# Optimization experiments

Hardware: AMD Instinct MI355X
Metric: run time of the kernel (lower is better)

Reference implementation:

```python
import jax, jax.numpy as jnp
import numpy as np


def setup_inputs() -> dict:
    key = jax.random.key(0)
    ks = jax.random.split(key, 6)
    B, C, H, W, Q = 16, 64, 64, 64, 8192
    HID = 256
    K = C * 9  # 576, unfolded channel count and srnet out_dim (co_mat=1)
    feat = jax.random.normal(ks[0], (B, C, H, W), jnp.float32)
    coord = jax.random.uniform(ks[1], (B, Q, 2), jnp.float32) * 2.0 - 1.0  # normalized [-1,1]
    cell = jnp.ones((B, Q, 2), jnp.float32) * (2.0 / 128.0)  # HR cell size for 128-px grid
    w1 = jax.random.normal(ks[2], (3, HID), jnp.float32) / np.sqrt(3.0)
    b1 = jnp.zeros((HID,), jnp.float32)
    w2 = jax.random.normal(ks[3], (HID, HID), jnp.float32) / np.sqrt(float(HID))
    b2 = jnp.zeros((HID,), jnp.float32)
    w3 = jax.random.normal(ks[4], (HID, K), jnp.float32) / np.sqrt(float(HID))
    b3 = jnp.zeros((K,), jnp.float32)
    return {"feat": feat, "coord": coord, "cell": cell,
            "w1": w1, "b1": b1, "w2": w2, "b2": b2, "w3": w3, "b3": b3}


def reference(feat, coord, cell, w1, b1, w2, b2, w3, b3):
    B, C, H, W = feat.shape
    Q = coord.shape[1]
    K = C * 9
    co_mat = 1
    # F.unfold(feat, 3, padding=1).view(B, C*9, H, W): channel-major, kernel pos minor
    padded = jnp.pad(feat, ((0, 0), (0, 0), (1, 1), (1, 1)))
    patches = jnp.stack([padded[:, :, i:i + H, j:j + W]
                         for i in range(3) for j in range(3)], axis=2)  # [B,C,9,H,W]
    featu = patches.reshape(B, K, H * W)
    # shift query coords by half a cell
    coord_ = coord - cell / 2.0
    coord_q = jnp.clip(coord_ + 1e-6, -1.0 + 1e-6, 1.0 - 1e-6)
    # nearest grid_sample, align_corners=False: idx = round(((c+1)*S - 1)/2)
    # coord[...,0] indexes H (grid y after flip), coord[...,1] indexes W (grid x)
    iy = jnp.clip(jnp.round(((coord_q[..., 0] + 1.0) * H - 1.0) / 2.0), 0, H - 1).astype(jnp.int32)
    ix = jnp.clip(jnp.round(((coord_q[..., 1] + 1.0) * W - 1.0) / 2.0), 0, W - 1).astype(jnp.int32)
    lin = iy * W + ix  # [B,Q]
    q_feat = jnp.take_along_axis(featu, lin[:, None, :], axis=2).transpose(0, 2, 1)  # [B,Q,K]
    # q_coord: make_coord value minus half-pixel shift at the nearest index = 2i/S - 1 (exact)
    qy = 2.0 * iy.astype(jnp.float32) / H - 1.0
    qx = 2.0 * ix.astype(jnp.float32) / W - 1.0
    rel_y = (coord_[..., 0] - qy) * (H / 2.0)
    rel_x = (coord_[..., 1] - qx) * (W / 2.0)
    r_rev = cell[..., 0] * (H / 2.0)
    inp = jnp.stack([rel_y, rel_x, r_rev], axis=-1)  # [B,Q,3]
    # srnet MLP: per-query filter of shape [K, co_mat]
    h = jax.nn.relu(inp @ w1 + b1)
    h = jax.nn.relu(h @ w2 + b2)
    wmat = (h @ w3 + b3).reshape(B, Q, K, co_mat)
    # bmm combine: [1,K] @ [K,co_mat] per query
    pred = jnp.einsum('bqk,bqkc->bqc', q_feat, wmat)  # [B,Q,1]
    return pred
```

## Files before the change

kernel.cpp:

```cpp
#include <hip/hip_runtime.h>
#include <hip/hip_bf16.h>

#define BB 16
#define CC 64
#define HH 64
#define WW 64
#define QQ 8192
#define HID 256
#define KK 576
#define HT 66
#define FROW 264

typedef short short8 __attribute__((ext_vector_type(8)));
typedef short sv4    __attribute__((ext_vector_type(4)));
typedef float f32x4  __attribute__((ext_vector_type(4)));

__device__ __forceinline__ short f2bf(float f) {
    union { float f; unsigned u; } v; v.f = f;
    unsigned r = v.u + 0x7fffu + ((v.u >> 16) & 1u);
    return (short)(r >> 16);
}
__device__ __forceinline__ float bf2f(short s) {
    union { unsigned u; float f; } v; v.u = ((unsigned)(unsigned short)s) << 16;
    return v.f;
}
__device__ __forceinline__ void barrier_lds() {
    asm volatile("s_waitcnt lgkmcnt(0)" ::: "memory");
    __builtin_amdgcn_s_barrier();
    asm volatile("" ::: "memory");
}
__device__ __forceinline__ void glld16(const short* g, short* l) {
    __builtin_amdgcn_global_load_lds(
        (const __attribute__((address_space(1))) void*)g,
        (__attribute__((address_space(3))) void*)l, 16, 0, 0);
}

__global__ __launch_bounds__(256) void prep_transpose_k(const float* __restrict__ feat,
                                                        const float* __restrict__ w2,
                                                        const float* __restrict__ w3,
                                                        const float* __restrict__ b3,
                                                        short* __restrict__ featT,
                                                        short* __restrict__ w3cB,
                                                        short* __restrict__ w2cB) {
    __shared__ float ftile[64][65];
    const int t = threadIdx.x;
    const int gidx = blockIdx.x * 256 + t;

    if (gidx < 156672) {
        int kchunk = gidx / 2176;
        int rem = gidx - kchunk * 2176;
        int n = rem >> 3, j = rem & 7;
        int kglob = kchunk * 8 + j;
        int pos = kglob >> 6, c = kglob & 63;
        float v = 0.f;
        if (n < 256)      v = w3[n * KK + c * 9 + pos];
        else if (n == 256) v = b3[c * 9 + pos];
        w3cB[gidx] = f2bf(v);
    }
    if (gidx < 65536) {
        int kchunk = gidx >> 11;
        int rem = gidx & 2047;
        int n = rem >> 3, j = rem & 7;
        int k = kchunk * 8 + j;
        w2cB[gidx] = f2bf(w2[k * 256 + n]);
    }

    const int b = blockIdx.x / HT;
    const int yy = blockIdx.x - b * HT;
    short* out_row = featT + ((b * HT + yy) * HT) * 64;

    if (yy == 0 || yy == HT - 1) {
        for (int idx = t; idx < HT * 64; idx += 256) out_row[idx] = 0;
        return;
    }
    const int y = yy - 1;
    const float* src = feat + ((b * CC) * HH + y) * WW;
#pragma unroll
    for (int i = 0; i < 16; ++i) {
        int idx = i * 256 + t;
        int c = idx >> 6, x = idx & 63;
        ftile[c][x] = src[c * (HH * WW) + x];
    }
    if (t < 64) out_row[t] = 0;
    else if (t < 128) out_row[(HT - 1) * 64 + (t - 64)] = 0;
    __syncthreads();
#pragma unroll
    for (int i = 0; i < 16; ++i) {
        int idx = i * 256 + t;
        int x = idx >> 6, c = idx & 63;
        out_row[(x + 1) * 64 + c] = f2bf(ftile[c][x]);
    }
}

#define SSTR 72
__global__ __launch_bounds__(256, 2) void conv_k(const short* __restrict__ featT,
                                                 const short* __restrict__ w3cB,
                                                 short* __restrict__ F) {
    __shared__ short slab[3 * HT * SSTR];
    __shared__ short Bb[2][8704];
    const int t = threadIdx.x;
    const int wave = t >> 6, lane = t & 63, quad = lane >> 4, ln16 = lane & 15;
    const int b = blockIdx.x >> 6, y = blockIdx.x & 63;

    f32x4 acc[4][5];
#pragma unroll
    for (int a = 0; a < 4; ++a)
#pragma unroll
        for (int i = 0; i < 5; ++i) acc[a][i] = (f32x4){0.f, 0.f, 0.f, 0.f};

    auto stageB = [&](int buf, int st) {
        const short* src = w3cB + st * 8704;
#pragma unroll
        for (int u = 0; u < 5; ++u) {
            int cidx = (u < 4) ? (u * 4 + wave) : 16;
            if (u < 4 || wave == 0)
                glld16(src + cidx * 512 + lane * 8, &Bb[buf][cidx * 512]);
        }
    };

    stageB(0, 0);

    const short* slabsrc = featT + b * (HT * HT * 64) + y * (HT * 64);
#pragma unroll
    for (int it = 0; it < 7; ++it) {
        int i = it * 256 + t;
        if (i < 1584) {
            short8 v = *(const short8*)(slabsrc + i * 8);
            int row = i >> 3, cs = (i & 7) * 8;
            *(short8*)(&slab[row * SSTR + cs]) = v;
        }
    }
    __syncthreads();

#pragma unroll
    for (int st = 0; st < 18; ++st) {
        const int cur = st & 1;
        if (st < 17) stageB(cur ^ 1, st + 1);
        const int pos = st >> 1, ks = st & 1;
        const int di = pos / 3, dj = pos - di * 3;
        short8 af[4];
#pragma unroll
        for (int ms = 0; ms < 4; ++ms)
            af[ms] = *(const short8*)(&slab[(di * HT + ms * 16 + ln16 + dj) * SSTR + ks * 32 + quad * 8]);
#pragma unroll
        for (int i = 0; i < 5; ++i) {
            int sub = (i < 4) ? (wave + 4 * i) : 16;
            short8 bf = *(const short8*)(&Bb[cur][(quad * 272 + sub * 16 + ln16) * 8]);
#pragma unroll
            for (int ms = 0; ms < 4; ++ms)
                acc[ms][i] = __builtin_amdgcn_mfma_f32_16x16x32_bf16(af[ms], bf, acc[ms][i], 0, 0, 0);
        }
        __syncthreads();
    }

#pragma unroll
    for (int h = 0; h < 2; ++h) {
#pragma unroll
        for (int i = 0; i < 5; ++i) {
            int sub = (i < 4) ? (wave + 4 * i) : 16;
            int n = sub * 16 + ln16;
            bool store = (i < 4) || (wave == 0 && n < FROW);
            if (store) {
#pragma unroll
                for (int ms2 = 0; ms2 < 2; ++ms2) {
                    int ms = h * 2 + ms2;
#pragma unroll
                    for (int r = 0; r < 4; ++r) {
                        int xl = ms2 * 16 + quad * 4 + r;
                        slab[xl * FROW + n] = f2bf(acc[ms][i][r]);
                    }
                }
            }
        }
        __syncthreads();
        short8* dst = (short8*)(F + ((long)(b * 64 + y) * 64 + h * 32) * FROW);
        const short8* src8 = (const short8*)slab;
#pragma unroll
        for (int it = 0; it < 5; ++it) {
            int idx = it * 256 + t;
            if (idx < (32 * FROW) / 8) dst[idx] = src8[idx];
        }
        __syncthreads();
    }
}

#define HSTR 264
__global__ __launch_bounds__(256, 3) void mlp_k(const float* __restrict__ coord,
                                                const float* __restrict__ cell,
                                                const float* __restrict__ w1,
                                                const float* __restrict__ b1,
                                                const float* __restrict__ b2v,
                                                const short* __restrict__ w2cB,
                                                const short* __restrict__ F,
                                                float* __restrict__ out) {
    __shared__ short Hh[64 * HSTR];
    __shared__ float red_s[64][4];

    const int t = threadIdx.x;
    const int wave = t >> 6, lane = t & 63, quad = lane >> 4, ln16 = lane & 15;
    const int qbase = blockIdx.x * 64;
    const int b = qbase >> 13;

    short8 wbuf[3][4];
    const short* w2base = w2cB + (quad * 256 + wave * 64 + ln16) * 8;
    auto loadW = [&](int s, int slot) {
#pragma unroll
        for (int i = 0; i < 4; ++i)
            wbuf[slot][i] = *(const short8*)(w2base + s * 8192 + i * 128);
    };

    const int g = qbase + lane;
    const float2 cc = *(const float2*)(coord + g * 2);
    const float2 ce = *(const float2*)(cell + g * 2);

    loadW(0, 0);
    loadW(1, 1);

    const float coy = cc.x - ce.x * 0.5f, cox = cc.y - ce.y * 0.5f;
    const float cqy = fminf(fmaxf(coy + 1e-6f, -0.999999f), 0.999999f);
    const float cqx = fminf(fmaxf(cox + 1e-6f, -0.999999f), 0.999999f);
    int iy = (int)rintf(((cqy + 1.0f) * 64.0f - 1.0f) * 0.5f); iy = min(max(iy, 0), 63);
    int ix = (int)rintf(((cqx + 1.0f) * 64.0f - 1.0f) * 0.5f); ix = min(max(ix, 0), 63);
    const int lin = iy * 64 + ix;
    const float in0 = (coy - ((float)iy * (1.0f / 32.0f) - 1.0f)) * 32.0f;
    const float in1 = (cox - ((float)ix * (1.0f / 32.0f) - 1.0f)) * 32.0f;
    const float in2 = ce.x * 32.0f;

    int linm[4];
#pragma unroll
    for (int ms = 0; ms < 4; ++ms) linm[ms] = __shfl(lin, ms * 16 + ln16, 64);

    short8 hv[8];
    const int k0w = wave * 64;
#pragma unroll
    for (int c8 = 0; c8 < 8; ++c8) {
        const int k0 = k0w + c8 * 8;
        f32x4 wa0 = *(const f32x4*)(w1 + k0),       wa1 = *(const f32x4*)(w1 + k0 + 4);
        f32x4 wb0 = *(const f32x4*)(w1 + 256 + k0), wb1 = *(const f32x4*)(w1 + 256 + k0 + 4);
        f32x4 wc0 = *(const f32x4*)(w1 + 512 + k0), wc1 = *(const f32x4*)(w1 + 512 + k0 + 4);
        f32x4 bb0 = *(const f32x4*)(b1 + k0),       bb1 = *(const f32x4*)(b1 + k0 + 4);
#pragma unroll
        for (int jj = 0; jj < 4; ++jj) {
            float v0 = fmaf(in0, wa0[jj], fmaf(in1, wb0[jj], fmaf(in2, wc0[jj], bb0[jj])));
            float v1 = fmaf(in0, wa1[jj], fmaf(in1, wb1[jj], fmaf(in2, wc1[jj], bb1[jj])));
            hv[c8][jj]     = f2bf(fmaxf(v0, 0.f));
            hv[c8][jj + 4] = f2bf(fmaxf(v1, 0.f));
        }
    }
#pragma unroll
    for (int c8 = 0; c8 < 8; ++c8)
        *(short8*)(&Hh[lane * HSTR + wave * 64 + c8 * 8]) = hv[c8];
    barrier_lds();

    const short* Fb = F + (long)b * 4096 * FROW;
    sv4 fv[4][4];
    short fbs = 0;
    f32x4 b2q[4];
    f32x4 acc2[4][4];
#pragma unroll
    for (int i = 0; i < 4; ++i)
#pragma unroll
        for (int ms = 0; ms < 4; ++ms) acc2[i][ms] = (f32x4){0.f, 0.f, 0.f, 0.f};

#pragma unroll
    for (int s = 0; s < 8; ++s) {
        if (s < 6) loadW(s + 2, (s + 2) % 3);
        short8 hf[4];
#pragma unroll
        for (int ms = 0; ms < 4; ++ms)
            hf[ms] = *(const short8*)(&Hh[(ms * 16 + ln16) * HSTR + s * 32 + quad * 8]);
        if (s == 6) {
#pragma unroll
            for (int ms = 0; ms < 4; ++ms) {
                const short* Fr = Fb + (long)linm[ms] * FROW + wave * 64 + quad * 4;
#pragma unroll
                for (int i = 0; i < 4; ++i) fv[ms][i] = *(const sv4*)(Fr + i * 16);
            }
            fbs = Fb[(long)lin * FROW + 256];
        }
        if (s == 7) {
#pragma unroll
            for (int i = 0; i < 4; ++i)
                b2q[i] = *(const f32x4*)(b2v + wave * 64 + i * 16 + quad * 4);
        }
#pragma unroll
        for (int i = 0; i < 4; ++i)
#pragma unroll
            for (int ms = 0; ms < 4; ++ms)
                acc2[i][ms] = __builtin_amdgcn_mfma_f32_16x16x32_bf16(wbuf[s % 3][i], hf[ms], acc2[i][ms], 0, 0, 0);
    }

    const float fbv = bf2f(fbs);
    float part[4] = {0.f, 0.f, 0.f, 0.f};
#pragma unroll
    for (int i = 0; i < 4; ++i)
#pragma unroll
        for (int ms = 0; ms < 4; ++ms)
#pragma unroll
            for (int r = 0; r < 4; ++r)
                part[ms] = fmaf(fmaxf(acc2[i][ms][r] + b2q[i][r], 0.f), bf2f(fv[ms][i][r]), part[ms]);
#pragma unroll
    for (int ms = 0; ms < 4; ++ms) {
        part[ms] += __shfl_xor(part[ms], 16, 64);
        part[ms] += __shfl_xor(part[ms], 32, 64);
    }
    if (quad == 0) {
#pragma unroll
        for (int ms = 0; ms < 4; ++ms) red_s[ms * 16 + ln16][wave] = part[ms];
    }
    barrier_lds();
    if (t < 64)
        out[qbase + t] = red_s[t][0] + red_s[t][1] + red_s[t][2] + red_s[t][3] + fbv;
}

extern "C" void kernel_launch(void* const* d_in, const int* in_sizes, int n_in,
                              void* d_out, int out_size, void* d_ws, size_t ws_size,
                              hipStream_t stream) {
    const float* feat  = (const float*)d_in[0];
    const float* coord = (const float*)d_in[1];
    const float* cell  = (const float*)d_in[2];
    const float* w1    = (const float*)d_in[3];
    const float* b1    = (const float*)d_in[4];
    const float* w2    = (const float*)d_in[5];
    const float* b2    = (const float*)d_in[6];
    const float* w3    = (const float*)d_in[7];
    const float* b3    = (const float*)d_in[8];
    float* out = (float*)d_out;

    char* ws = (char*)d_ws;
    short* w3cB  = (short*)(ws);
    short* w2cB  = (short*)(ws + 313344);
    short* featT = (short*)(ws + 444416);
    short* F     = (short*)(ws + 9365504);
    (void)ws_size; (void)in_sizes; (void)n_in; (void)out_size;

    prep_transpose_k<<<BB * HT, 256, 0, stream>>>(feat, w2, w3, b3, featT, w3cB, w2cB);
    conv_k<<<BB * HH, 256, 0, stream>>>(featT, w3cB, F);
    mlp_k<<<(BB * QQ) / 64, 256, 0, stream>>>(coord, cell, w1, b1, b2, w2cB, F, out);
}
```

Before: 150.9 us.

## Load conv B operand straight into registers with triple-buffered prefetch

In the conv kernel, the w3-derived B fragments are no longer staged through a double-buffered LDS array via global_load_lds. Each lane now loads its own short8 fragments from global memory into a three-slot register ring, prefetching two stages ahead. This removes the per-stage __syncthreads and about 35 KB of LDS per block. The cost is roughly 60 extra VGPRs, which risks spills under the two-blocks-per-SM launch bound. Dropping the last main-loop barrier also leaves a possible race: a wave may start writing the epilogue into slab while another wave is still reading its final A fragments from slab.

```diff
diff --git a/kernel.cpp b/kernel.cpp
--- a/kernel.cpp
+++ b/kernel.cpp
@@ -28,11 +28,6 @@
     asm volatile("s_waitcnt lgkmcnt(0)" ::: "memory");
     __builtin_amdgcn_s_barrier();
     asm volatile("" ::: "memory");
-}
-__device__ __forceinline__ void glld16(const short* g, short* l) {
-    __builtin_amdgcn_global_load_lds(
-        (const __attribute__((address_space(1))) void*)g,
-        (__attribute__((address_space(3))) void*)l, 16, 0, 0);
 }
 
 __global__ __launch_bounds__(256) void prep_transpose_k(const float* __restrict__ feat,
@@ -97,7 +92,6 @@
                                                  const short* __restrict__ w3cB,
                                                  short* __restrict__ F) {
     __shared__ short slab[3 * HT * SSTR];
-    __shared__ short Bb[2][8704];
     const int t = threadIdx.x;
     const int wave = t >> 6, lane = t & 63, quad = lane >> 4, ln16 = lane & 15;
     const int b = blockIdx.x >> 6, y = blockIdx.x & 63;
@@ -108,17 +102,18 @@
 #pragma unroll
         for (int i = 0; i < 5; ++i) acc[a][i] = (f32x4){0.f, 0.f, 0.f, 0.f};
 
-    auto stageB = [&](int buf, int st) {
-        const short* src = w3cB + st * 8704;
-#pragma unroll
-        for (int u = 0; u < 5; ++u) {
-            int cidx = (u < 4) ? (u * 4 + wave) : 16;
-            if (u < 4 || wave == 0)
-                glld16(src + cidx * 512 + lane * 8, &Bb[buf][cidx * 512]);
+    short8 bbuf[3][5];
+    const short* bbase = w3cB + (quad * 272 + ln16) * 8;
+    auto loadB = [&](int st, int slot) {
+#pragma unroll
+        for (int i = 0; i < 5; ++i) {
+            int sub = (i < 4) ? (wave + 4 * i) : 16;
+            bbuf[slot][i] = *(const short8*)(bbase + st * 8704 + sub * 128);
         }
     };
 
-    stageB(0, 0);
+    loadB(0, 0);
+    loadB(1, 1);
 
     const short* slabsrc = featT + b * (HT * HT * 64) + y * (HT * 64);
 #pragma unroll
@@ -130,12 +125,11 @@
             *(short8*)(&slab[row * SSTR + cs]) = v;
         }
     }
-    __syncthreads();
+    barrier_lds();
 
 #pragma unroll
     for (int st = 0; st < 18; ++st) {
-        const int cur = st & 1;
-        if (st < 17) stageB(cur ^ 1, st + 1);
+        if (st < 16) loadB(st + 2, (st + 2) % 3);
         const int pos = st >> 1, ks = st & 1;
         const int di = pos / 3, dj = pos - di * 3;
         short8 af[4];
@@ -143,18 +137,15 @@
         for (int ms = 0; ms < 4; ++ms)
             af[ms] = *(const short8*)(&slab[(di * HT + ms * 16 + ln16 + dj) * SSTR + ks * 32 + quad * 8]);
 #pragma unroll
-        for (int i = 0; i < 5; ++i) {
-            int sub = (i < 4) ? (wave + 4 * i) : 16;
-            short8 bf = *(const short8*)(&Bb[cur][(quad * 272 + sub * 16 + ln16) * 8]);
+        for (int i = 0; i < 5; ++i)
 #pragma unroll
             for (int ms = 0; ms < 4; ++ms)
-                acc[ms][i] = __builtin_amdgcn_mfma_f32_16x16x32_bf16(af[ms], bf, acc[ms][i], 0, 0, 0);
-        }
-        __syncthreads();
+                acc[ms][i] = __builtin_amdgcn_mfma_f32_16x16x32_bf16(af[ms], bbuf[st % 3][i], acc[ms][i], 0, 0, 0);
     }
 
 #pragma unroll
     for (int h = 0; h < 2; ++h) {
+        if (h) barrier_lds();
 #pragma unroll
         for (int i = 0; i < 5; ++i) {
             int sub = (i < 4) ? (wave + 4 * i) : 16;
@@ -172,7 +163,7 @@
                 }
             }
         }
-        __syncthreads();
+        barrier_lds();
         short8* dst = (short8*)(F + ((long)(b * 64 + y) * 64 + h * 32) * FROW);
         const short8* src8 = (const short8*)slab;
 #pragma unroll
@@ -180,7 +171,6 @@
             int idx = it * 256 + t;
             if (idx < (32 * FROW) / 8) dst[idx] = src8[idx];
         }
-        __syncthreads();
     }
 }
 
```

Result: no change. 152.2 us (+0.9%).
